# Kernel optimization log

Measured on AMD Instinct MI355X. Metric: run time of the kernel, lower is better.

The kernel has to match this reference:

```python
import jax, jax.numpy as jnp
import numpy as np

VOCAB, H, HEADS, S, FF = 100, 8, 2, 6, 16
HD = H // HEADS  # head_dim = 4
EPS = 1e-5


def _layernorm(x, g, b):
    mu = jnp.mean(x, axis=-1, keepdims=True)
    var = jnp.mean((x - mu) ** 2, axis=-1, keepdims=True)
    return (x - mu) * jax.lax.rsqrt(var + EPS) * g + b


def setup_inputs() -> dict:
    key = jax.random.key(0)
    ks = jax.random.split(key, 20)
    B = 262144
    d = {
        'input_ids': jax.random.randint(ks[0], (B, S), 0, VOCAB),
        'tok_emb': jax.random.normal(ks[1], (VOCAB, H), jnp.float32) * 0.02,
        'pos_emb': jax.random.normal(ks[2], (S, H), jnp.float32) * 0.02,
        'Wq': jax.random.normal(ks[3], (H, H), jnp.float32) * 0.1,
        'bq': jnp.zeros((H,), jnp.float32),
        'Wk': jax.random.normal(ks[4], (H, H), jnp.float32) * 0.1,
        'bk': jnp.zeros((H,), jnp.float32),
        'Wv': jax.random.normal(ks[5], (H, H), jnp.float32) * 0.1,
        'bv': jnp.zeros((H,), jnp.float32),
        'Wo': jax.random.normal(ks[6], (H, H), jnp.float32) * 0.1,
        'bo': jnp.zeros((H,), jnp.float32),
        'W1': jax.random.normal(ks[7], (FF, H), jnp.float32) * 0.1,
        'b1': jnp.zeros((FF,), jnp.float32),
        'W2': jax.random.normal(ks[8], (H, FF), jnp.float32) * 0.1,
        'b2': jnp.zeros((H,), jnp.float32),
        'g1': jnp.ones((H,), jnp.float32),
        'be1': jnp.zeros((H,), jnp.float32),
        'g2': jnp.ones((H,), jnp.float32),
        'be2': jnp.zeros((H,), jnp.float32),
    }
    return d


def reference(input_ids, tok_emb, pos_emb, Wq, bq, Wk, bk, Wv, bv, Wo, bo,
              W1, b1, W2, b2, g1, be1, g2, be2):
    B, Sq = input_ids.shape
    x = tok_emb[input_ids] + pos_emb[None, :, :]  # [B,S,H]
    q = x @ Wq.T + bq
    k = x @ Wk.T + bk
    v = x @ Wv.T + bv
    # split heads: [B, heads, S, head_dim]
    q = q.reshape(B, Sq, HEADS, HD).transpose(0, 2, 1, 3)
    k = k.reshape(B, Sq, HEADS, HD).transpose(0, 2, 1, 3)
    v = v.reshape(B, Sq, HEADS, HD).transpose(0, 2, 1, 3)
    scores = jnp.einsum('bhsd,bhtd->bhst', q, k) / (HD ** 0.5)
    probs = jax.nn.softmax(scores, axis=-1)
    attn = jnp.einsum('bhst,bhtd->bhsd', probs, v)
    attn = attn.transpose(0, 2, 1, 3).reshape(B, Sq, H)
    attn = attn @ Wo.T + bo
    h = _layernorm(x + attn, g1, be1)
    ffn = jax.nn.gelu(h @ W1.T + b1, approximate=False) @ W2.T + b2
    return _layernorm(h + ffn, g2, be2)
```

## Files before the change

kernel.cpp:

```cpp
#include <hip/hip_runtime.h>

#define TT_S 6
#define TT_H 8
#define TT_FF 16
#define SEQ_PER_BLK 64
#define BLK 384
#define KV_STRIDE_U 52

#define WQH  0
#define WKH  32
#define WVH  64
#define WOH  96
#define W1H  128
#define W2H  192
#define POSH 256

typedef __fp16   h2_t  __attribute__((ext_vector_type(2)));
typedef __fp16   h8_t  __attribute__((ext_vector_type(8)));
typedef _Float16 f16x2 __attribute__((ext_vector_type(2)));

__device__ __forceinline__ unsigned pk2(float a, float b) {
  h2_t h = __builtin_amdgcn_cvt_pkrtz(a, b);
  return __builtin_bit_cast(unsigned, h);
}
__device__ __forceinline__ h2_t pk2h(float a, float b) {
  return __builtin_amdgcn_cvt_pkrtz(a, b);
}
__device__ __forceinline__ h2_t bch(unsigned u) {
  return __builtin_bit_cast(h2_t, u);
}

#if __has_builtin(__builtin_amdgcn_fdot2)
__device__ __forceinline__ float dot2f(h2_t a, h2_t b, float c) {
  return __builtin_amdgcn_fdot2(__builtin_bit_cast(f16x2, a),
                                __builtin_bit_cast(f16x2, b), c, false);
}
#else
__device__ __forceinline__ float dot2f(h2_t a, h2_t b, float c) {
  return fmaf((float)a[0], (float)b[0], fmaf((float)a[1], (float)b[1], c));
}
#endif

__global__ void tt_prep(const float* __restrict__ Wq, const float* __restrict__ Wk,
                        const float* __restrict__ Wv, const float* __restrict__ Wo,
                        const float* __restrict__ W1, const float* __restrict__ W2,
                        const float* __restrict__ pos, unsigned* __restrict__ ws)
{
  const int i = threadIdx.x;
  if (i < 128) {
    const float* Wm = (i < 32) ? Wq : (i < 64) ? Wk : (i < 96) ? Wv : Wo;
    const int p = i & 31;
    ws[i] = pk2(Wm[2*p], Wm[2*p+1]);
  }
  if (i < 64) {
    ws[W1H + i] = pk2(W1[2*i], W1[2*i+1]);
    ws[W2H + i] = pk2(W2[2*i], W2[2*i+1]);
  }
  if (i < 24) ws[POSH + i] = pk2(pos[2*i], pos[2*i+1]);
}

__global__ __launch_bounds__(BLK, 6) void tt_fused(
    const int* __restrict__ ids,
    const float* __restrict__ tok_emb,
    const unsigned* __restrict__ wsu,
    const float* __restrict__ bq, const float* __restrict__ bk,
    const float* __restrict__ bv, const float* __restrict__ bo,
    const float* __restrict__ b1, const float* __restrict__ b2,
    const float* __restrict__ g1, const float* __restrict__ be1,
    const float* __restrict__ g2, const float* __restrict__ be2,
    float* __restrict__ out, int B)
{
  __shared__ __align__(16) unsigned s_kv[SEQ_PER_BLK * KV_STRIDE_U];
  __shared__ __align__(16) unsigned s_tok[400];

  const int tid = threadIdx.x;
  for (int i = tid; i < 400; i += BLK) {
    float2 tv = ((const float2*)tok_emb)[i];
    s_tok[i] = pk2(tv.x, tv.y);
  }
  __syncthreads();

  const int s_loc = tid / TT_S;
  const int t     = tid - s_loc * TT_S;
  const int seq_g = blockIdx.x * SEQ_PER_BLK + s_loc;
  const bool valid = (seq_g < B);
  const size_t gidx = (size_t)blockIdx.x * BLK + tid;
  const int id = valid ? ids[gidx] : 0;

  uint4 tw = ((const uint4*)s_tok)[id];
  uint4 pw = ((const uint4*)(wsu + POSH))[t];
  h2_t xs0 = bch(tw.x) + bch(pw.x);
  h2_t xs1 = bch(tw.y) + bch(pw.y);
  h2_t xs2 = bch(tw.z) + bch(pw.z);
  h2_t xs3 = bch(tw.w) + bch(pw.w);

  float xf[TT_H];
  xf[0] = (float)xs0[0]; xf[1] = (float)xs0[1];
  xf[2] = (float)xs1[0]; xf[3] = (float)xs1[1];
  xf[4] = (float)xs2[0]; xf[5] = (float)xs2[1];
  xf[6] = (float)xs3[0]; xf[7] = (float)xs3[1];

  {
    float kr[TT_H], vr[TT_H];
    #pragma unroll
    for (int i = 0; i < TT_H; ++i) {
      float ak = bk[i], av = bv[i];
      ak = dot2f(xs0, bch(wsu[WKH + i*4 + 0]), ak);
      ak = dot2f(xs1, bch(wsu[WKH + i*4 + 1]), ak);
      ak = dot2f(xs2, bch(wsu[WKH + i*4 + 2]), ak);
      ak = dot2f(xs3, bch(wsu[WKH + i*4 + 3]), ak);
      av = dot2f(xs0, bch(wsu[WVH + i*4 + 0]), av);
      av = dot2f(xs1, bch(wsu[WVH + i*4 + 1]), av);
      av = dot2f(xs2, bch(wsu[WVH + i*4 + 2]), av);
      av = dot2f(xs3, bch(wsu[WVH + i*4 + 3]), av);
      kr[i] = ak; vr[i] = av;
    }
    unsigned* kvp = s_kv + s_loc * KV_STRIDE_U + t * 8;
    uint4 w0, w1;
    w0.x = pk2(kr[0], kr[1]); w0.y = pk2(kr[2], kr[3]);
    w0.z = pk2(kr[4], kr[5]); w0.w = pk2(kr[6], kr[7]);
    w1.x = pk2(vr[0], vr[1]); w1.y = pk2(vr[2], vr[3]);
    w1.z = pk2(vr[4], vr[5]); w1.w = pk2(vr[6], vr[7]);
    ((uint4*)kvp)[0] = w0;
    ((uint4*)kvp)[1] = w1;
  }
  __syncthreads();

  h2_t qh[4];
  #pragma unroll
  for (int i = 0; i < 4; ++i) {
    float a0 = bq[2*i], a1 = bq[2*i+1];
    a0 = dot2f(xs0, bch(wsu[WQH + (2*i)*4 + 0]), a0);
    a0 = dot2f(xs1, bch(wsu[WQH + (2*i)*4 + 1]), a0);
    a0 = dot2f(xs2, bch(wsu[WQH + (2*i)*4 + 2]), a0);
    a0 = dot2f(xs3, bch(wsu[WQH + (2*i)*4 + 3]), a0);
    a1 = dot2f(xs0, bch(wsu[WQH + (2*i+1)*4 + 0]), a1);
    a1 = dot2f(xs1, bch(wsu[WQH + (2*i+1)*4 + 1]), a1);
    a1 = dot2f(xs2, bch(wsu[WQH + (2*i+1)*4 + 2]), a1);
    a1 = dot2f(xs3, bch(wsu[WQH + (2*i+1)*4 + 3]), a1);
    qh[i] = pk2h(a0 * 0.7213475204f, a1 * 0.7213475204f);
  }

  float acc[TT_H] = {0.f,0.f,0.f,0.f,0.f,0.f,0.f,0.f};
  float sum0 = 0.f, sum1 = 0.f;
  const uint4* kvb = (const uint4*)(s_kv + s_loc * KV_STRIDE_U);
  #pragma unroll
  for (int t2 = 0; t2 < TT_S; ++t2) {
    uint4 kw = kvb[t2*2];
    uint4 vw = kvb[t2*2+1];
    float d0 = dot2f(qh[0], bch(kw.x), 0.f);
    d0 = dot2f(qh[1], bch(kw.y), d0);
    float d1 = dot2f(qh[2], bch(kw.z), 0.f);
    d1 = dot2f(qh[3], bch(kw.w), d1);
    float e0 = __builtin_amdgcn_exp2f(d0);
    float e1 = __builtin_amdgcn_exp2f(d1);
    sum0 += e0; sum1 += e1;
    h8_t vh = __builtin_bit_cast(h8_t, vw);
    acc[0] = fmaf(e0, (float)vh[0], acc[0]);
    acc[1] = fmaf(e0, (float)vh[1], acc[1]);
    acc[2] = fmaf(e0, (float)vh[2], acc[2]);
    acc[3] = fmaf(e0, (float)vh[3], acc[3]);
    acc[4] = fmaf(e1, (float)vh[4], acc[4]);
    acc[5] = fmaf(e1, (float)vh[5], acc[5]);
    acc[6] = fmaf(e1, (float)vh[6], acc[6]);
    acc[7] = fmaf(e1, (float)vh[7], acc[7]);
  }
  h2_t ah[4];
  {
    float inv0 = __builtin_amdgcn_rcpf(sum0);
    float inv1 = __builtin_amdgcn_rcpf(sum1);
    ah[0] = pk2h(acc[0]*inv0, acc[1]*inv0);
    ah[1] = pk2h(acc[2]*inv0, acc[3]*inv0);
    ah[2] = pk2h(acc[4]*inv1, acc[5]*inv1);
    ah[3] = pk2h(acc[6]*inv1, acc[7]*inv1);
  }

  float r[TT_H];
  float mu = 0.f;
  #pragma unroll
  for (int i = 0; i < TT_H; ++i) {
    float o = bo[i];
    o = dot2f(ah[0], bch(wsu[WOH + i*4 + 0]), o);
    o = dot2f(ah[1], bch(wsu[WOH + i*4 + 1]), o);
    o = dot2f(ah[2], bch(wsu[WOH + i*4 + 2]), o);
    o = dot2f(ah[3], bch(wsu[WOH + i*4 + 3]), o);
    r[i] = xf[i] + o;
    mu += r[i];
  }
  mu *= 0.125f;
  float var = 0.f;
  #pragma unroll
  for (int i = 0; i < TT_H; ++i) { float d = r[i] - mu; var = fmaf(d, d, var); }
  float rin = __builtin_amdgcn_rsqf(fmaf(var, 0.125f, 1e-5f));
  float mc = mu * rin;
  float hr[TT_H];
  #pragma unroll
  for (int i = 0; i < TT_H; ++i)
    hr[i] = fmaf(fmaf(r[i], rin, -mc), g1[i], be1[i]);
  h2_t hh[4];
  hh[0] = pk2h(hr[0], hr[1]);
  hh[1] = pk2h(hr[2], hr[3]);
  hh[2] = pk2h(hr[4], hr[5]);
  hh[3] = pk2h(hr[6], hr[7]);

  h2_t fh[8];
  #pragma unroll
  for (int f = 0; f < TT_FF; f += 2) {
    float u0 = b1[f], u1 = b1[f+1];
    u0 = dot2f(hh[0], bch(wsu[W1H + f*4 + 0]), u0);
    u0 = dot2f(hh[1], bch(wsu[W1H + f*4 + 1]), u0);
    u0 = dot2f(hh[2], bch(wsu[W1H + f*4 + 2]), u0);
    u0 = dot2f(hh[3], bch(wsu[W1H + f*4 + 3]), u0);
    u1 = dot2f(hh[0], bch(wsu[W1H + f*4 + 4]), u1);
    u1 = dot2f(hh[1], bch(wsu[W1H + f*4 + 5]), u1);
    u1 = dot2f(hh[2], bch(wsu[W1H + f*4 + 6]), u1);
    u1 = dot2f(hh[3], bch(wsu[W1H + f*4 + 7]), u1);
    float e0 = __builtin_amdgcn_exp2f(u0 * fmaf(0.1029432f, u0*u0, 2.3022072f));
    float e1 = __builtin_amdgcn_exp2f(u1 * fmaf(0.1029432f, u1*u1, 2.3022072f));
    float g0 = fmaf(-u0, __builtin_amdgcn_rcpf(e0 + 1.0f), u0);
    float g1v = fmaf(-u1, __builtin_amdgcn_rcpf(e1 + 1.0f), u1);
    fh[f>>1] = pk2h(g0, g1v);
  }

  float r2[TT_H];
  float mu2 = 0.f;
  #pragma unroll
  for (int i = 0; i < TT_H; ++i) {
    float y = b2[i];
    y = dot2f(fh[0], bch(wsu[W2H + i*8 + 0]), y);
    y = dot2f(fh[1], bch(wsu[W2H + i*8 + 1]), y);
    y = dot2f(fh[2], bch(wsu[W2H + i*8 + 2]), y);
    y = dot2f(fh[3], bch(wsu[W2H + i*8 + 3]), y);
    y = dot2f(fh[4], bch(wsu[W2H + i*8 + 4]), y);
    y = dot2f(fh[5], bch(wsu[W2H + i*8 + 5]), y);
    y = dot2f(fh[6], bch(wsu[W2H + i*8 + 6]), y);
    y = dot2f(fh[7], bch(wsu[W2H + i*8 + 7]), y);
    r2[i] = hr[i] + y;
    mu2 += r2[i];
  }
  mu2 *= 0.125f;
  float var2 = 0.f;
  #pragma unroll
  for (int i = 0; i < TT_H; ++i) { float d = r2[i] - mu2; var2 = fmaf(d, d, var2); }
  float rin2 = __builtin_amdgcn_rsqf(fmaf(var2, 0.125f, 1e-5f));
  float mc2 = mu2 * rin2;

  if (valid) {
    float res[TT_H];
    #pragma unroll
    for (int i = 0; i < TT_H; ++i)
      res[i] = fmaf(fmaf(r2[i], rin2, -mc2), g2[i], be2[i]);
    float* op = out + gidx * TT_H;
    float4 v0; v0.x = res[0]; v0.y = res[1]; v0.z = res[2]; v0.w = res[3];
    float4 v1; v1.x = res[4]; v1.y = res[5]; v1.z = res[6]; v1.w = res[7];
    ((float4*)op)[0] = v0;
    ((float4*)op)[1] = v1;
  }
}

extern "C" void kernel_launch(void* const* d_in, const int* in_sizes, int n_in,
                              void* d_out, int out_size, void* d_ws, size_t ws_size,
                              hipStream_t stream) {
  const int*   ids = (const int*)  d_in[0];
  const float* tok = (const float*)d_in[1];
  const float* pos = (const float*)d_in[2];
  const float* Wq  = (const float*)d_in[3];
  const float* bq  = (const float*)d_in[4];
  const float* Wk  = (const float*)d_in[5];
  const float* bk  = (const float*)d_in[6];
  const float* Wv  = (const float*)d_in[7];
  const float* bv  = (const float*)d_in[8];
  const float* Wo  = (const float*)d_in[9];
  const float* bo  = (const float*)d_in[10];
  const float* W1  = (const float*)d_in[11];
  const float* b1  = (const float*)d_in[12];
  const float* W2  = (const float*)d_in[13];
  const float* b2  = (const float*)d_in[14];
  const float* g1  = (const float*)d_in[15];
  const float* be1 = (const float*)d_in[16];
  const float* g2  = (const float*)d_in[17];
  const float* be2 = (const float*)d_in[18];
  float* out = (float*)d_out;
  unsigned* ws = (unsigned*)d_ws;

  hipLaunchKernelGGL(tt_prep, dim3(1), dim3(128), 0, stream,
                     Wq, Wk, Wv, Wo, W1, W2, pos, ws);

  const int B = in_sizes[0] / TT_S;
  const int grid = (B + SEQ_PER_BLK - 1) / SEQ_PER_BLK;
  hipLaunchKernelGGL(tt_fused, dim3(grid), dim3(BLK), 0, stream,
                     ids, tok, ws, bq, bk, bv, bo, b1, b2,
                     g1, be1, g2, be2, out, B);
}
```

Measured before the change: 144.1 us.

## Map sequences to single waves, use wave barriers, and prepack token table

Each wavefront now owns 10 whole sequences (60 of 64 lanes active), so the K/V exchange through shared memory needs only a wave barrier instead of a block-wide __syncthreads. The per-block token-embedding conversion into LDS is moved into the prep kernel, which writes a packed fp16 table to the workspace that is then read from global/L2. Blocks shrink to 256 threads with a higher occupancy hint. The cost is about 6% idle lanes per wave and token gathers that go through cache instead of LDS.

```diff
diff --git a/kernel.cpp b/kernel.cpp
--- a/kernel.cpp
+++ b/kernel.cpp
@@ -3,9 +3,12 @@
 #define TT_S 6
 #define TT_H 8
 #define TT_FF 16
-#define SEQ_PER_BLK 64
-#define BLK 384
-#define KV_STRIDE_U 52
+#define WAVES_PER_BLK 4
+#define BLK (WAVES_PER_BLK * 64)
+#define SEQ_PER_WAVE 10
+#define SEQ_PER_BLK (WAVES_PER_BLK * SEQ_PER_WAVE)
+#define SEQ_STRIDE_U 52
+#define WAVE_STRIDE_U (SEQ_PER_WAVE * SEQ_STRIDE_U + 8)
 
 #define WQH  0
 #define WKH  32
@@ -14,6 +17,7 @@
 #define W1H  128
 #define W2H  192
 #define POSH 256
+#define TOKH 288
 
 typedef __fp16   h2_t  __attribute__((ext_vector_type(2)));
 typedef __fp16   h8_t  __attribute__((ext_vector_type(8)));
@@ -44,7 +48,8 @@
 __global__ void tt_prep(const float* __restrict__ Wq, const float* __restrict__ Wk,
                         const float* __restrict__ Wv, const float* __restrict__ Wo,
                         const float* __restrict__ W1, const float* __restrict__ W2,
-                        const float* __restrict__ pos, unsigned* __restrict__ ws)
+                        const float* __restrict__ pos, const float* __restrict__ tok,
+                        unsigned* __restrict__ ws)
 {
   const int i = threadIdx.x;
   if (i < 128) {
@@ -57,11 +62,11 @@
     ws[W2H + i] = pk2(W2[2*i], W2[2*i+1]);
   }
   if (i < 24) ws[POSH + i] = pk2(pos[2*i], pos[2*i+1]);
-}
-
-__global__ __launch_bounds__(BLK, 6) void tt_fused(
+  if (i < 400) ws[TOKH + i] = pk2(tok[2*i], tok[2*i+1]);
+}
+
+__global__ __launch_bounds__(BLK, 8) void tt_fused(
     const int* __restrict__ ids,
-    const float* __restrict__ tok_emb,
     const unsigned* __restrict__ wsu,
     const float* __restrict__ bq, const float* __restrict__ bk,
     const float* __restrict__ bv, const float* __restrict__ bo,
@@ -70,24 +75,20 @@
     const float* __restrict__ g2, const float* __restrict__ be2,
     float* __restrict__ out, int B)
 {
-  __shared__ __align__(16) unsigned s_kv[SEQ_PER_BLK * KV_STRIDE_U];
-  __shared__ __align__(16) unsigned s_tok[400];
+  __shared__ __align__(16) unsigned s_kv[WAVES_PER_BLK * WAVE_STRIDE_U];
 
   const int tid = threadIdx.x;
-  for (int i = tid; i < 400; i += BLK) {
-    float2 tv = ((const float2*)tok_emb)[i];
-    s_tok[i] = pk2(tv.x, tv.y);
-  }
-  __syncthreads();
-
-  const int s_loc = tid / TT_S;
-  const int t     = tid - s_loc * TT_S;
-  const int seq_g = blockIdx.x * SEQ_PER_BLK + s_loc;
-  const bool valid = (seq_g < B);
-  const size_t gidx = (size_t)blockIdx.x * BLK + tid;
-  const int id = valid ? ids[gidx] : 0;
-
-  uint4 tw = ((const uint4*)s_tok)[id];
+  const int wv  = tid >> 6;
+  const int ln  = tid & 63;
+  const int slr = ln / 6;
+  const int t   = ln - slr * 6;
+  const int seq_g = blockIdx.x * SEQ_PER_BLK + wv * SEQ_PER_WAVE + slr;
+  if (ln >= 60 || seq_g >= B) return;
+
+  const size_t gidx = (size_t)seq_g * TT_S + t;
+  const int id = ids[gidx];
+
+  uint4 tw = ((const uint4*)(wsu + TOKH))[id];
   uint4 pw = ((const uint4*)(wsu + POSH))[t];
   h2_t xs0 = bch(tw.x) + bch(pw.x);
   h2_t xs1 = bch(tw.y) + bch(pw.y);
@@ -99,6 +100,8 @@
   xf[2] = (float)xs1[0]; xf[3] = (float)xs1[1];
   xf[4] = (float)xs2[0]; xf[5] = (float)xs2[1];
   xf[6] = (float)xs3[0]; xf[7] = (float)xs3[1];
+
+  unsigned* kvbase = s_kv + wv * WAVE_STRIDE_U + slr * SEQ_STRIDE_U;
 
   {
     float kr[TT_H], vr[TT_H];
@@ -115,7 +118,7 @@
       av = dot2f(xs3, bch(wsu[WVH + i*4 + 3]), av);
       kr[i] = ak; vr[i] = av;
     }
-    unsigned* kvp = s_kv + s_loc * KV_STRIDE_U + t * 8;
+    unsigned* kvp = kvbase + t * 8;
     uint4 w0, w1;
     w0.x = pk2(kr[0], kr[1]); w0.y = pk2(kr[2], kr[3]);
     w0.z = pk2(kr[4], kr[5]); w0.w = pk2(kr[6], kr[7]);
@@ -124,7 +127,7 @@
     ((uint4*)kvp)[0] = w0;
     ((uint4*)kvp)[1] = w1;
   }
-  __syncthreads();
+  __builtin_amdgcn_wave_barrier();
 
   h2_t qh[4];
   #pragma unroll
@@ -143,7 +146,7 @@
 
   float acc[TT_H] = {0.f,0.f,0.f,0.f,0.f,0.f,0.f,0.f};
   float sum0 = 0.f, sum1 = 0.f;
-  const uint4* kvb = (const uint4*)(s_kv + s_loc * KV_STRIDE_U);
+  const uint4* kvb = (const uint4*)kvbase;
   #pragma unroll
   for (int t2 = 0; t2 < TT_S; ++t2) {
     uint4 kw = kvb[t2*2];
@@ -245,17 +248,15 @@
   float rin2 = __builtin_amdgcn_rsqf(fmaf(var2, 0.125f, 1e-5f));
   float mc2 = mu2 * rin2;
 
-  if (valid) {
-    float res[TT_H];
-    #pragma unroll
-    for (int i = 0; i < TT_H; ++i)
-      res[i] = fmaf(fmaf(r2[i], rin2, -mc2), g2[i], be2[i]);
-    float* op = out + gidx * TT_H;
-    float4 v0; v0.x = res[0]; v0.y = res[1]; v0.z = res[2]; v0.w = res[3];
-    float4 v1; v1.x = res[4]; v1.y = res[5]; v1.z = res[6]; v1.w = res[7];
-    ((float4*)op)[0] = v0;
-    ((float4*)op)[1] = v1;
-  }
+  float res[TT_H];
+  #pragma unroll
+  for (int i = 0; i < TT_H; ++i)
+    res[i] = fmaf(fmaf(r2[i], rin2, -mc2), g2[i], be2[i]);
+  float* op = out + gidx * TT_H;
+  float4 v0; v0.x = res[0]; v0.y = res[1]; v0.z = res[2]; v0.w = res[3];
+  float4 v1; v1.x = res[4]; v1.y = res[5]; v1.z = res[6]; v1.w = res[7];
+  ((float4*)op)[0] = v0;
+  ((float4*)op)[1] = v1;
 }
 
 extern "C" void kernel_launch(void* const* d_in, const int* in_sizes, int n_in,
@@ -283,12 +284,12 @@
   float* out = (float*)d_out;
   unsigned* ws = (unsigned*)d_ws;
 
-  hipLaunchKernelGGL(tt_prep, dim3(1), dim3(128), 0, stream,
-                     Wq, Wk, Wv, Wo, W1, W2, pos, ws);
+  hipLaunchKernelGGL(tt_prep, dim3(1), dim3(512), 0, stream,
+                     Wq, Wk, Wv, Wo, W1, W2, pos, tok, ws);
 
   const int B = in_sizes[0] / TT_S;
   const int grid = (B + SEQ_PER_BLK - 1) / SEQ_PER_BLK;
   hipLaunchKernelGGL(tt_fused, dim3(grid), dim3(BLK), 0, stream,
-                     ids, tok, ws, bq, bk, bv, bo, b1, b2,
+                     ids, ws, bq, bk, bv, bo, b1, b2,
                      g1, be1, g2, be2, out, B);
 }
```

Result: faster. 139.5 us (-3.2%).
